# Kernel tuning notes

Measured on AMD Instinct MI355X. Metric: run time of the kernel, lower is better.

## Reference

```python
import jax, jax.numpy as jnp
import numpy as np

BN_EPS = 1e-5


def setup_inputs() -> dict:
    key = jax.random.key(0)
    k1, k2, k3 = jax.random.split(key, 3)
    N, C_IN, C_OUT, B = 1_000_000, 64, 128, 16
    features = jax.random.normal(k1, (N, C_IN), dtype=jnp.float32)
    weight = jax.random.normal(k2, (C_OUT, C_IN), dtype=jnp.float32) * (1.0 / np.sqrt(C_IN))
    gamma = jnp.ones((C_OUT,), dtype=jnp.float32)
    beta = jnp.zeros((C_OUT,), dtype=jnp.float32)
    indices = jnp.sort(jax.random.randint(k3, (N,), 0, B)).astype(jnp.int64)
    return {"features": features, "weight": weight, "gamma": gamma,
            "beta": beta, "indices": indices, "num_segments": B}


def reference(features, weight, gamma, beta, indices, num_segments):
    # scatter-mean: [N, C_in] -> [B, C_in]
    seg_sum = jax.ops.segment_sum(features, indices, num_segments=num_segments)
    counts = jax.ops.segment_sum(jnp.ones((features.shape[0], 1), features.dtype),
                                 indices, num_segments=num_segments)
    pooled = seg_sum / jnp.maximum(counts, 1.0)
    # Linear (no bias): [B, C_in] @ [C_in, C_out]
    h = pooled @ weight.T
    # BatchNorm1d (training-mode batch statistics, biased variance)
    mean = jnp.mean(h, axis=0)
    var = jnp.mean((h - mean) ** 2, axis=0)
    h = (h - mean) * jax.lax.rsqrt(var + BN_EPS) * gamma + beta
    # ReLU then gather back to every point: [B, C_out] -> [N, C_out]
    h = jnp.maximum(h, 0.0)
    return h[indices]
```

## Files before the change

kernel.cpp:

```cpp
#include <hip/hip_runtime.h>

#define NSEG 16
#define CIN 64
#define COUT 128
#define BN_EPS 1e-5f

typedef float vf4 __attribute__((ext_vector_type(4)));

__device__ __forceinline__ bool idx_is64(const void* p, int N) {
    return ((const int*)p)[N - 1] == 0;
}
__device__ __forceinline__ int load_idx(const void* p, long long i, bool is64) {
    return is64 ? (int)((const long long*)p)[i] : ((const int*)p)[i];
}


__global__ __launch_bounds__(256) void k_zero(float* __restrict__ seg_sum) {
    for (int i = threadIdx.x; i < NSEG * CIN; i += 256) seg_sum[i] = 0.0f;
}

__global__ __launch_bounds__(256) void k_segsum(const float* __restrict__ feat,
                                                const void* __restrict__ idx,
                                                float* __restrict__ seg_sum,
                                                int N, int rows_per_blk) {
    __shared__ float acc_lds[NSEG * CIN];
    const int tid = threadIdx.x;
    for (int i = tid; i < NSEG * CIN; i += 256) acc_lds[i] = 0.0f;
    __syncthreads();

    const bool is64 = idx_is64(idx, N);
    const int q4 = (tid & 15) * 4;
    const int row0 = blockIdx.x * rows_per_blk;
    const int row_end = min(row0 + rows_per_blk, N);

    vf4 acc = {0.f, 0.f, 0.f, 0.f};
    int cur = -1;
    for (int r = row0 + (tid >> 4); r < row_end; r += 16) {
        const int s = load_idx(idx, r, is64);
        if (s != cur) {
            if (cur >= 0) {
                atomicAdd(&acc_lds[cur * CIN + q4 + 0], acc.x);
                atomicAdd(&acc_lds[cur * CIN + q4 + 1], acc.y);
                atomicAdd(&acc_lds[cur * CIN + q4 + 2], acc.z);
                atomicAdd(&acc_lds[cur * CIN + q4 + 3], acc.w);
            }
            acc = (vf4){0.f, 0.f, 0.f, 0.f};
            cur = s;
        }
        const vf4 v = *(const vf4*)(feat + (size_t)r * CIN + q4);
        acc += v;
    }
    if (cur >= 0) {
        atomicAdd(&acc_lds[cur * CIN + q4 + 0], acc.x);
        atomicAdd(&acc_lds[cur * CIN + q4 + 1], acc.y);
        atomicAdd(&acc_lds[cur * CIN + q4 + 2], acc.z);
        atomicAdd(&acc_lds[cur * CIN + q4 + 3], acc.w);
    }
    __syncthreads();
    for (int i = tid; i < NSEG * CIN; i += 256) {
        const float v = acc_lds[i];
        if (v != 0.0f) atomicAdd(&seg_sum[i], v);
    }
}

__global__ __launch_bounds__(256) void k_mlp(const float* __restrict__ seg_sum,
                                             const void* __restrict__ idx, int N,
                                             const float* __restrict__ W,
                                             const float* __restrict__ gamma,
                                             const float* __restrict__ beta,
                                             float* __restrict__ h_final) {
    __shared__ float pooled[NSEG * CIN];
    __shared__ float h_lds[NSEG * COUT];
    __shared__ float cnt[NSEG];
    __shared__ float scale_s[COUT], bias_s[COUT];
    __shared__ int bnd[NSEG + 1];
    const int tid = threadIdx.x;
    const bool is64 = idx_is64(idx, N);

    if (tid <= NSEG) {
        if (tid == 0) bnd[0] = 0;
        else if (tid == NSEG) bnd[NSEG] = N;
        else {
            int lo = 0, hi = N;
            while (lo < hi) {
                const int mid = (lo + hi) >> 1;
                if (load_idx(idx, mid, is64) < tid) lo = mid + 1; else hi = mid;
            }
            bnd[tid] = lo;
        }
    }
    __syncthreads();
    if (tid < NSEG) cnt[tid] = (float)max(bnd[tid + 1] - bnd[tid], 1);
    __syncthreads();
    for (int i = tid; i < NSEG * CIN; i += 256) pooled[i] = seg_sum[i] / cnt[i / CIN];
    __syncthreads();

    const int co = tid & 127;
    const int half = tid >> 7;
    float w[CIN];
    #pragma unroll
    for (int c = 0; c < CIN; c += 4)
        *(vf4*)(w + c) = *(const vf4*)(W + (size_t)co * CIN + c);
    for (int b = half; b < NSEG; b += 2) {
        float a = 0.f;
        #pragma unroll
        for (int c = 0; c < CIN; ++c) a += pooled[b * CIN + c] * w[c];
        h_lds[b * COUT + co] = a;
    }
    __syncthreads();

    if (tid < COUT) {
        float m = 0.f;
        #pragma unroll
        for (int b = 0; b < NSEG; ++b) m += h_lds[b * COUT + tid];
        m *= (1.0f / NSEG);
        float v = 0.f;
        #pragma unroll
        for (int b = 0; b < NSEG; ++b) {
            const float d = h_lds[b * COUT + tid] - m;
            v += d * d;
        }
        v *= (1.0f / NSEG);
        const float sc = gamma[tid] * rsqrtf(v + BN_EPS);
        scale_s[tid] = sc;
        bias_s[tid] = beta[tid] - m * sc;
    }
    __syncthreads();
    for (int b = half; b < NSEG; b += 2) {
        const float hv = h_lds[b * COUT + co] * scale_s[co] + bias_s[co];
        h_final[b * COUT + co] = fmaxf(hv, 0.0f);
    }
}

__global__ __launch_bounds__(256) void k_gather(const float* __restrict__ h_final,
                                                const void* __restrict__ idx,
                                                float* __restrict__ out, int N) {
    __shared__ vf4 h4[NSEG * 32];
    const int tid = threadIdx.x;
    for (int i = tid; i < NSEG * 32; i += 256) h4[i] = ((const vf4*)h_final)[i];
    const bool is64 = idx_is64(idx, N);
    __syncthreads();

    vf4* out4 = (vf4*)out;
    const long long total = (long long)N * 32;
    const long long stride = (long long)gridDim.x * 256;
    for (long long i = (long long)blockIdx.x * 256 + tid; i < total; i += stride) {
        const int row = (int)(i >> 5);
        const int q = (int)(i & 31);
        const int s = load_idx(idx, row, is64);
        __builtin_nontemporal_store(h4[s * 32 + q], &out4[i]);
    }
}

extern "C" void kernel_launch(void* const* d_in, const int* in_sizes, int n_in,
                              void* d_out, int out_size, void* d_ws, size_t ws_size,
                              hipStream_t stream) {
    const float* feat  = (const float*)d_in[0];
    const float* W     = (const float*)d_in[1];
    const float* gamma = (const float*)d_in[2];
    const float* beta  = (const float*)d_in[3];
    const void*  idx   = d_in[4];
    const int N = in_sizes[4];

    float* seg_sum = (float*)d_ws;
    float* h_final = (float*)d_ws + NSEG * CIN;

    hipLaunchKernelGGL(k_zero, dim3(1), dim3(256), 0, stream, seg_sum);

    const int NB = 1024;
    const int rows_per_blk = (((N + NB - 1) / NB) + 15) & ~15;
    hipLaunchKernelGGL(k_segsum, dim3(NB), dim3(256), 0, stream,
                       feat, idx, seg_sum, N, rows_per_blk);

    hipLaunchKernelGGL(k_mlp, dim3(1), dim3(256), 0, stream,
                       seg_sum, idx, N, W, gamma, beta, h_final);

    hipLaunchKernelGGL(k_gather, dim3(2048), dim3(256), 0, stream,
                       h_final, idx, (float*)d_out, N);
}
```

Before: 155.8 us.

## Compute segment boundaries once and drop per-row index reads

Moves the binary search for segment boundaries into the first kernel, which also zeroes the accumulator, and stores the boundaries in workspace. The segment-sum and gather kernels then walk each block's row range by segment using those boundaries instead of loading the int64 index per row. This removes the index-array traffic (about 8 MB per pass) and the per-row branching from both large kernels. The cost is a serial binary search on the critical path before the reduction, and a gather split into contiguous row chunks per block.

Result: slower. 163.1 us (+4.7%).

```diff
diff --git a/kernel.cpp b/kernel.cpp
--- a/kernel.cpp
+++ b/kernel.cpp
@@ -15,46 +15,57 @@
 }
 
 
-__global__ __launch_bounds__(256) void k_zero(float* __restrict__ seg_sum) {
-    for (int i = threadIdx.x; i < NSEG * CIN; i += 256) seg_sum[i] = 0.0f;
+__global__ __launch_bounds__(256) void k_bounds(const void* __restrict__ idx, int N,
+                                                float* __restrict__ seg_sum,
+                                                int* __restrict__ bnd) {
+    const int tid = threadIdx.x;
+    for (int i = tid; i < NSEG * CIN; i += 256) seg_sum[i] = 0.0f;
+    if (tid <= NSEG) {
+        if (tid == 0) bnd[0] = 0;
+        else if (tid == NSEG) bnd[NSEG] = N;
+        else {
+            const bool is64 = idx_is64(idx, N);
+            int lo = 0, hi = N;
+            while (lo < hi) {
+                const int mid = (lo + hi) >> 1;
+                if (load_idx(idx, mid, is64) < tid) lo = mid + 1; else hi = mid;
+            }
+            bnd[tid] = lo;
+        }
+    }
 }
 
 __global__ __launch_bounds__(256) void k_segsum(const float* __restrict__ feat,
-                                                const void* __restrict__ idx,
+                                                const int* __restrict__ bnd,
                                                 float* __restrict__ seg_sum,
                                                 int N, int rows_per_blk) {
     __shared__ float acc_lds[NSEG * CIN];
+    __shared__ int sbnd[NSEG + 1];
     const int tid = threadIdx.x;
+    if (tid <= NSEG) sbnd[tid] = bnd[tid];
     for (int i = tid; i < NSEG * CIN; i += 256) acc_lds[i] = 0.0f;
     __syncthreads();
 
-    const bool is64 = idx_is64(idx, N);
-    const int q4 = (tid & 15) * 4;
     const int row0 = blockIdx.x * rows_per_blk;
     const int row_end = min(row0 + rows_per_blk, N);
-
-    vf4 acc = {0.f, 0.f, 0.f, 0.f};
-    int cur = -1;
-    for (int r = row0 + (tid >> 4); r < row_end; r += 16) {
-        const int s = load_idx(idx, r, is64);
-        if (s != cur) {
-            if (cur >= 0) {
-                atomicAdd(&acc_lds[cur * CIN + q4 + 0], acc.x);
-                atomicAdd(&acc_lds[cur * CIN + q4 + 1], acc.y);
-                atomicAdd(&acc_lds[cur * CIN + q4 + 2], acc.z);
-                atomicAdd(&acc_lds[cur * CIN + q4 + 3], acc.w);
-            }
-            acc = (vf4){0.f, 0.f, 0.f, 0.f};
-            cur = s;
+    if (row0 < row_end) {
+        const int q4 = (tid & 15) * 4;
+        const int lr = tid >> 4;
+        int s = 0;
+        while (s < NSEG - 1 && sbnd[s + 1] <= row0) ++s;
+        for (; s < NSEG && sbnd[s] < row_end; ++s) {
+            const int a = max(sbnd[s], row0);
+            const int b = min(sbnd[s + 1], row_end);
+            if (a >= b) continue;
+            vf4 acc = {0.f, 0.f, 0.f, 0.f};
+            #pragma unroll 4
+            for (int r = a + lr; r < b; r += 16)
+                acc += *(const vf4*)(feat + (size_t)r * CIN + q4);
+            atomicAdd(&acc_lds[s * CIN + q4 + 0], acc.x);
+            atomicAdd(&acc_lds[s * CIN + q4 + 1], acc.y);
+            atomicAdd(&acc_lds[s * CIN + q4 + 2], acc.z);
+            atomicAdd(&acc_lds[s * CIN + q4 + 3], acc.w);
         }
-        const vf4 v = *(const vf4*)(feat + (size_t)r * CIN + q4);
-        acc += v;
-    }
-    if (cur >= 0) {
-        atomicAdd(&acc_lds[cur * CIN + q4 + 0], acc.x);
-        atomicAdd(&acc_lds[cur * CIN + q4 + 1], acc.y);
-        atomicAdd(&acc_lds[cur * CIN + q4 + 2], acc.z);
-        atomicAdd(&acc_lds[cur * CIN + q4 + 3], acc.w);
     }
     __syncthreads();
     for (int i = tid; i < NSEG * CIN; i += 256) {
@@ -64,7 +75,7 @@
 }
 
 __global__ __launch_bounds__(256) void k_mlp(const float* __restrict__ seg_sum,
-                                             const void* __restrict__ idx, int N,
+                                             const int* __restrict__ bnd,
                                              const float* __restrict__ W,
                                              const float* __restrict__ gamma,
                                              const float* __restrict__ beta,
@@ -73,23 +84,8 @@
     __shared__ float h_lds[NSEG * COUT];
     __shared__ float cnt[NSEG];
     __shared__ float scale_s[COUT], bias_s[COUT];
-    __shared__ int bnd[NSEG + 1];
     const int tid = threadIdx.x;
-    const bool is64 = idx_is64(idx, N);
 
-    if (tid <= NSEG) {
-        if (tid == 0) bnd[0] = 0;
-        else if (tid == NSEG) bnd[NSEG] = N;
-        else {
-            int lo = 0, hi = N;
-            while (lo < hi) {
-                const int mid = (lo + hi) >> 1;
-                if (load_idx(idx, mid, is64) < tid) lo = mid + 1; else hi = mid;
-            }
-            bnd[tid] = lo;
-        }
-    }
-    __syncthreads();
     if (tid < NSEG) cnt[tid] = (float)max(bnd[tid + 1] - bnd[tid], 1);
     __syncthreads();
     for (int i = tid; i < NSEG * CIN; i += 256) pooled[i] = seg_sum[i] / cnt[i / CIN];
@@ -133,22 +129,31 @@
 }
 
 __global__ __launch_bounds__(256) void k_gather(const float* __restrict__ h_final,
-                                                const void* __restrict__ idx,
-                                                float* __restrict__ out, int N) {
+                                                const int* __restrict__ bnd,
+                                                float* __restrict__ out,
+                                                int N, int rows_per_blk) {
     __shared__ vf4 h4[NSEG * 32];
+    __shared__ int sbnd[NSEG + 1];
     const int tid = threadIdx.x;
+    if (tid <= NSEG) sbnd[tid] = bnd[tid];
     for (int i = tid; i < NSEG * 32; i += 256) h4[i] = ((const vf4*)h_final)[i];
-    const bool is64 = idx_is64(idx, N);
     __syncthreads();
 
+    const int row0 = blockIdx.x * rows_per_blk;
+    const int row_end = min(row0 + rows_per_blk, N);
+    if (row0 >= row_end) return;
+
+    const int q = tid & 31;
+    const int rofs = tid >> 5;
+    int r = row0 + rofs;
+    int s = 0;
+    while (s < NSEG - 1 && sbnd[s + 1] <= r) ++s;
+    vf4 pat = h4[s * 32 + q];
+    int nb = sbnd[s + 1];
     vf4* out4 = (vf4*)out;
-    const long long total = (long long)N * 32;
-    const long long stride = (long long)gridDim.x * 256;
-    for (long long i = (long long)blockIdx.x * 256 + tid; i < total; i += stride) {
-        const int row = (int)(i >> 5);
-        const int q = (int)(i & 31);
-        const int s = load_idx(idx, row, is64);
-        __builtin_nontemporal_store(h4[s * 32 + q], &out4[i]);
+    for (; r < row_end; r += 8) {
+        while (r >= nb) { ++s; nb = sbnd[s + 1]; pat = h4[s * 32 + q]; }
+        __builtin_nontemporal_store(pat, &out4[(size_t)r * 32 + q]);
     }
 }
 
@@ -164,17 +169,21 @@
 
     float* seg_sum = (float*)d_ws;
     float* h_final = (float*)d_ws + NSEG * CIN;
+    int*   bnd     = (int*)((float*)d_ws + NSEG * CIN + NSEG * COUT);
 
-    hipLaunchKernelGGL(k_zero, dim3(1), dim3(256), 0, stream, seg_sum);
+    hipLaunchKernelGGL(k_bounds, dim3(1), dim3(256), 0, stream, idx, N, seg_sum, bnd);
 
-    const int NB = 1024;
-    const int rows_per_blk = (((N + NB - 1) / NB) + 15) & ~15;
-    hipLaunchKernelGGL(k_segsum, dim3(NB), dim3(256), 0, stream,
-                       feat, idx, seg_sum, N, rows_per_blk);
+    const int NB1 = 1024;
+    const int rpb1 = (((N + NB1 - 1) / NB1) + 15) & ~15;
+    hipLaunchKernelGGL(k_segsum, dim3(NB1), dim3(256), 0, stream,
+                       feat, bnd, seg_sum, N, rpb1);
 
     hipLaunchKernelGGL(k_mlp, dim3(1), dim3(256), 0, stream,
-                       seg_sum, idx, N, W, gamma, beta, h_final);
+                       seg_sum, bnd, W, gamma, beta, h_final);
 
-    hipLaunchKernelGGL(k_gather, dim3(2048), dim3(256), 0, stream,
-                       h_final, idx, (float*)d_out, N);
+    const int NB2 = 2048;
+    const int rpb2 = (((N + NB2 - 1) / NB2) + 7) & ~7;
+    const int nb2 = (N + rpb2 - 1) / rpb2;
+    hipLaunchKernelGGL(k_gather, dim3(nb2), dim3(256), 0, stream,
+                       h_final, bnd, (float*)d_out, N, rpb2);
 }
```

## Fuse MLP into segment-sum via last-block completion and skip index loads in uniform blocks

Applied to the files above, without the earlier changes.

The separate zero and MLP kernels are removed. The segment-sum kernel now also counts rows per segment, and the last block to finish (found through an atomic done counter) computes pooled means, the linear layer, batchnorm and ReLU. This drops the binary-search pass and two kernel launches. Blocks whose first and last index match skip per-row index loads in both segsum and gather, and gather now works on contiguous row ranges per block. The cost is extra LDS in every segsum block, which may reduce occupancy, plus a serialized single-block tail at the end of the segsum kernel.

After: 225.9 us. +45.0%, slower.

```diff
diff --git a/kernel.cpp b/kernel.cpp
--- a/kernel.cpp
+++ b/kernel.cpp
@@ -15,100 +15,115 @@
 }
 
 
-__global__ __launch_bounds__(256) void k_zero(float* __restrict__ seg_sum) {
-    for (int i = threadIdx.x; i < NSEG * CIN; i += 256) seg_sum[i] = 0.0f;
-}
-
-__global__ __launch_bounds__(256) void k_segsum(const float* __restrict__ feat,
-                                                const void* __restrict__ idx,
-                                                float* __restrict__ seg_sum,
-                                                int N, int rows_per_blk) {
+__global__ __launch_bounds__(256) void k_segsum(
+    const float* __restrict__ feat, const void* __restrict__ idxp,
+    const float* __restrict__ W, const float* __restrict__ gamma,
+    const float* __restrict__ beta,
+    float* __restrict__ seg_sum, int* __restrict__ gcnt, int* __restrict__ done,
+    float* __restrict__ h_final, int N, int rows_per_blk)
+{
     __shared__ float acc_lds[NSEG * CIN];
+    __shared__ int   cnt_lds[NSEG];
+    __shared__ float h_lds[NSEG * COUT];
+    __shared__ float scale_s[COUT], bias_s[COUT];
+    __shared__ int   lastflag;
+
     const int tid = threadIdx.x;
     for (int i = tid; i < NSEG * CIN; i += 256) acc_lds[i] = 0.0f;
-    __syncthreads();
-
-    const bool is64 = idx_is64(idx, N);
-    const int q4 = (tid & 15) * 4;
+    if (tid < NSEG) cnt_lds[tid] = 0;
+    __syncthreads();
+
+    const bool is64 = idx_is64(idxp, N);
     const int row0 = blockIdx.x * rows_per_blk;
     const int row_end = min(row0 + rows_per_blk, N);
-
-    vf4 acc = {0.f, 0.f, 0.f, 0.f};
-    int cur = -1;
-    for (int r = row0 + (tid >> 4); r < row_end; r += 16) {
-        const int s = load_idx(idx, r, is64);
-        if (s != cur) {
+    const int q  = tid & 15;
+    const int rp = tid >> 4;
+    const vf4* feat4 = (const vf4*)feat;
+
+    if (row0 < row_end) {
+        const int s0 = load_idx(idxp, row0, is64);
+        const int s1 = load_idx(idxp, row_end - 1, is64);
+        if (s0 == s1) {
+            vf4 acc = {0.f, 0.f, 0.f, 0.f};
+            #pragma unroll 4
+            for (int r = row0 + rp; r < row_end; r += 16)
+                acc += feat4[(size_t)r * 16 + q];
+            atomicAdd(&acc_lds[s0 * CIN + q * 4 + 0], acc.x);
+            atomicAdd(&acc_lds[s0 * CIN + q * 4 + 1], acc.y);
+            atomicAdd(&acc_lds[s0 * CIN + q * 4 + 2], acc.z);
+            atomicAdd(&acc_lds[s0 * CIN + q * 4 + 3], acc.w);
+            if (tid == 0) cnt_lds[s0] = row_end - row0;
+        } else {
+            vf4 acc = {0.f, 0.f, 0.f, 0.f};
+            int cur = -1, run = 0;
+            for (int r = row0 + rp; r < row_end; r += 16) {
+                const int s = load_idx(idxp, r, is64);
+                if (s != cur) {
+                    if (cur >= 0) {
+                        atomicAdd(&acc_lds[cur * CIN + q * 4 + 0], acc.x);
+                        atomicAdd(&acc_lds[cur * CIN + q * 4 + 1], acc.y);
+                        atomicAdd(&acc_lds[cur * CIN + q * 4 + 2], acc.z);
+                        atomicAdd(&acc_lds[cur * CIN + q * 4 + 3], acc.w);
+                        if (q == 0) atomicAdd(&cnt_lds[cur], run);
+                    }
+                    acc = (vf4){0.f, 0.f, 0.f, 0.f};
+                    run = 0; cur = s;
+                }
+                acc += feat4[(size_t)r * 16 + q];
+                ++run;
+            }
             if (cur >= 0) {
-                atomicAdd(&acc_lds[cur * CIN + q4 + 0], acc.x);
-                atomicAdd(&acc_lds[cur * CIN + q4 + 1], acc.y);
-                atomicAdd(&acc_lds[cur * CIN + q4 + 2], acc.z);
-                atomicAdd(&acc_lds[cur * CIN + q4 + 3], acc.w);
+                atomicAdd(&acc_lds[cur * CIN + q * 4 + 0], acc.x);
+                atomicAdd(&acc_lds[cur * CIN + q * 4 + 1], acc.y);
+                atomicAdd(&acc_lds[cur * CIN + q * 4 + 2], acc.z);
+                atomicAdd(&acc_lds[cur * CIN + q * 4 + 3], acc.w);
+                if (q == 0) atomicAdd(&cnt_lds[cur], run);
             }
-            acc = (vf4){0.f, 0.f, 0.f, 0.f};
-            cur = s;
         }
-        const vf4 v = *(const vf4*)(feat + (size_t)r * CIN + q4);
-        acc += v;
-    }
-    if (cur >= 0) {
-        atomicAdd(&acc_lds[cur * CIN + q4 + 0], acc.x);
-        atomicAdd(&acc_lds[cur * CIN + q4 + 1], acc.y);
-        atomicAdd(&acc_lds[cur * CIN + q4 + 2], acc.z);
-        atomicAdd(&acc_lds[cur * CIN + q4 + 3], acc.w);
     }
     __syncthreads();
     for (int i = tid; i < NSEG * CIN; i += 256) {
         const float v = acc_lds[i];
         if (v != 0.0f) atomicAdd(&seg_sum[i], v);
     }
-}
-
-__global__ __launch_bounds__(256) void k_mlp(const float* __restrict__ seg_sum,
-                                             const void* __restrict__ idx, int N,
-                                             const float* __restrict__ W,
-                                             const float* __restrict__ gamma,
-                                             const float* __restrict__ beta,
-                                             float* __restrict__ h_final) {
-    __shared__ float pooled[NSEG * CIN];
-    __shared__ float h_lds[NSEG * COUT];
-    __shared__ float cnt[NSEG];
-    __shared__ float scale_s[COUT], bias_s[COUT];
-    __shared__ int bnd[NSEG + 1];
-    const int tid = threadIdx.x;
-    const bool is64 = idx_is64(idx, N);
-
-    if (tid <= NSEG) {
-        if (tid == 0) bnd[0] = 0;
-        else if (tid == NSEG) bnd[NSEG] = N;
-        else {
-            int lo = 0, hi = N;
-            while (lo < hi) {
-                const int mid = (lo + hi) >> 1;
-                if (load_idx(idx, mid, is64) < tid) lo = mid + 1; else hi = mid;
-            }
-            bnd[tid] = lo;
-        }
-    }
-    __syncthreads();
-    if (tid < NSEG) cnt[tid] = (float)max(bnd[tid + 1] - bnd[tid], 1);
-    __syncthreads();
-    for (int i = tid; i < NSEG * CIN; i += 256) pooled[i] = seg_sum[i] / cnt[i / CIN];
-    __syncthreads();
-
-    const int co = tid & 127;
-    const int half = tid >> 7;
-    float w[CIN];
+    if (tid < NSEG && cnt_lds[tid] != 0) atomicAdd(&gcnt[tid], cnt_lds[tid]);
+    __syncthreads();
+
+    if (tid == 0) {
+        __threadfence();
+        const int old = atomicAdd(done, 1);
+        lastflag = (old == (int)gridDim.x - 1);
+    }
+    __syncthreads();
+    if (!lastflag) return;
+
+    __threadfence();
+    if (tid < NSEG) {
+        const int c = __hip_atomic_load(&gcnt[tid], __ATOMIC_RELAXED,
+                                        __HIP_MEMORY_SCOPE_AGENT);
+        cnt_lds[tid] = max(c, 1);
+    }
+    __syncthreads();
+    for (int i = tid; i < NSEG * CIN; i += 256) {
+        const float v = __hip_atomic_load(&seg_sum[i], __ATOMIC_RELAXED,
+                                          __HIP_MEMORY_SCOPE_AGENT);
+        acc_lds[i] = v / (float)cnt_lds[i >> 6];
+    }
+    __syncthreads();
+
+    const vf4* W4 = (const vf4*)W;
+    const vf4* P4 = (const vf4*)acc_lds;
     #pragma unroll
-    for (int c = 0; c < CIN; c += 4)
-        *(vf4*)(w + c) = *(const vf4*)(W + (size_t)co * CIN + c);
-    for (int b = half; b < NSEG; b += 2) {
-        float a = 0.f;
+    for (int k = 0; k < 8; ++k) {
+        const int o = tid + k * 256;
+        const int b = o >> 7, co = o & 127;
+        vf4 s4 = {0.f, 0.f, 0.f, 0.f};
         #pragma unroll
-        for (int c = 0; c < CIN; ++c) a += pooled[b * CIN + c] * w[c];
-        h_lds[b * COUT + co] = a;
-    }
-    __syncthreads();
-
+        for (int c4 = 0; c4 < 16; ++c4)
+            s4 += W4[co * 16 + c4] * P4[b * 16 + c4];
+        h_lds[o] = s4.x + s4.y + s4.z + s4.w;
+    }
+    __syncthreads();
     if (tid < COUT) {
         float m = 0.f;
         #pragma unroll
@@ -126,29 +141,45 @@
         bias_s[tid] = beta[tid] - m * sc;
     }
     __syncthreads();
-    for (int b = half; b < NSEG; b += 2) {
-        const float hv = h_lds[b * COUT + co] * scale_s[co] + bias_s[co];
-        h_final[b * COUT + co] = fmaxf(hv, 0.0f);
-    }
-}
-
-__global__ __launch_bounds__(256) void k_gather(const float* __restrict__ h_final,
-                                                const void* __restrict__ idx,
-                                                float* __restrict__ out, int N) {
+    #pragma unroll
+    for (int k = 0; k < 8; ++k) {
+        const int o = tid + k * 256;
+        const int co = o & 127;
+        h_final[o] = fmaxf(h_lds[o] * scale_s[co] + bias_s[co], 0.0f);
+    }
+}
+
+__global__ __launch_bounds__(256) void k_gather(
+    const float* __restrict__ h_final, const void* __restrict__ idxp,
+    float* __restrict__ out, int N, int rows_per_blk)
+{
     __shared__ vf4 h4[NSEG * 32];
     const int tid = threadIdx.x;
     for (int i = tid; i < NSEG * 32; i += 256) h4[i] = ((const vf4*)h_final)[i];
-    const bool is64 = idx_is64(idx, N);
-    __syncthreads();
-
+    __syncthreads();
+
+    const int row0 = blockIdx.x * rows_per_blk;
+    const int row_end = min(row0 + rows_per_blk, N);
+    if (row0 >= row_end) return;
+    const bool is64 = idx_is64(idxp, N);
+    const int q = tid & 31;
+    const int rofs = tid >> 5;
     vf4* out4 = (vf4*)out;
-    const long long total = (long long)N * 32;
-    const long long stride = (long long)gridDim.x * 256;
-    for (long long i = (long long)blockIdx.x * 256 + tid; i < total; i += stride) {
-        const int row = (int)(i >> 5);
-        const int q = (int)(i & 31);
-        const int s = load_idx(idx, row, is64);
-        __builtin_nontemporal_store(h4[s * 32 + q], &out4[i]);
+
+    const int s0 = load_idx(idxp, row0, is64);
+    const int s1 = load_idx(idxp, row_end - 1, is64);
+    if (s0 == s1) {
+        const vf4 pat = h4[s0 * 32 + q];
+        #pragma unroll 4
+        for (int r = row0 + rofs; r < row_end; r += 8)
+            __builtin_nontemporal_store(pat, &out4[(size_t)r * 32 + q]);
+    } else {
+        int cur = -1; vf4 pat = {0.f, 0.f, 0.f, 0.f};
+        for (int r = row0 + rofs; r < row_end; r += 8) {
+            const int s = load_idx(idxp, r, is64);
+            if (s != cur) { pat = h4[s * 32 + q]; cur = s; }
+            __builtin_nontemporal_store(pat, &out4[(size_t)r * 32 + q]);
+        }
     }
 }
 
@@ -163,18 +194,21 @@
     const int N = in_sizes[4];
 
     float* seg_sum = (float*)d_ws;
-    float* h_final = (float*)d_ws + NSEG * CIN;
-
-    hipLaunchKernelGGL(k_zero, dim3(1), dim3(256), 0, stream, seg_sum);
-
-    const int NB = 1024;
-    const int rows_per_blk = (((N + NB - 1) / NB) + 15) & ~15;
-    hipLaunchKernelGGL(k_segsum, dim3(NB), dim3(256), 0, stream,
-                       feat, idx, seg_sum, N, rows_per_blk);
-
-    hipLaunchKernelGGL(k_mlp, dim3(1), dim3(256), 0, stream,
-                       seg_sum, idx, N, W, gamma, beta, h_final);
-
-    hipLaunchKernelGGL(k_gather, dim3(2048), dim3(256), 0, stream,
-                       h_final, idx, (float*)d_out, N);
-}
+    int*   gcnt    = (int*)d_ws + 1024;
+    int*   done    = (int*)d_ws + 1040;
+    float* h_final = (float*)d_ws + 1056;
+
+    hipMemsetAsync(d_ws, 0, 1041 * sizeof(int), stream);
+
+    const int NB = 2048;
+    const int rpb1 = (((N + NB - 1) / NB) + 15) & ~15;
+    const int nb1 = (N + rpb1 - 1) / rpb1;
+    hipLaunchKernelGGL(k_segsum, dim3(nb1), dim3(256), 0, stream,
+                       feat, idx, W, gamma, beta, seg_sum, gcnt, done,
+                       h_final, N, rpb1);
+
+    const int rpb2 = (((N + NB - 1) / NB) + 7) & ~7;
+    const int nb2 = (N + rpb2 - 1) / rpb2;
+    hipLaunchKernelGGL(k_gather, dim3(nb2), dim3(256), 0, stream,
+                       h_final, idx, (float*)d_out, N, rpb2);
+}
```
